# Optimization experiments

Hardware: AMD Instinct MI355X
Metric: run time of the kernel (lower is better)

## Reference

```python
import jax, jax.numpy as jnp
import numpy as np

EMBED_DIM = 1024
K_DIM = 64
NUM_HEADS = 16


def setup_inputs() -> dict:
    key = jax.random.key(0)
    kx, kq, kk, kv, kw = jax.random.split(key, 5)
    x = jax.random.normal(kx, (4, 2048, EMBED_DIM), dtype=jnp.float32)
    # per-head weights stacked along a leading head axis (torch.randn init)
    wq = jax.random.normal(kq, (NUM_HEADS, EMBED_DIM, K_DIM), dtype=jnp.float32)
    wk = jax.random.normal(kk, (NUM_HEADS, EMBED_DIM, K_DIM), dtype=jnp.float32)
    wv = jax.random.normal(kv, (NUM_HEADS, EMBED_DIM, K_DIM), dtype=jnp.float32)
    w = jax.random.normal(kw, (NUM_HEADS * K_DIM, EMBED_DIM), dtype=jnp.float32)
    return {"x": x, "wq": wq, "wk": wk, "wv": wv, "w": w}


def reference(x, wq, wk, wv, w):
    # x: [B,S,D]; wq/wk/wv: [H,D,K]; w: [H*K, D]
    q = jnp.einsum('bsd,hdk->bhsk', x, wq)
    k = jnp.einsum('bsd,hdk->bhsk', x, wk)
    v = jnp.einsum('bsd,hdk->bhsk', x, wv)
    scale = 1.0 / jnp.sqrt(jnp.asarray(K_DIM, x.dtype))
    scores = jnp.einsum('bhsk,bhtk->bhst', q, k) * scale  # [B,H,S,S]
    attn = jax.nn.softmax(scores, axis=-1)
    ctx = jnp.einsum('bhst,bhtk->bhsk', attn, v)  # [B,H,S,K]
    B, H, S, K = ctx.shape
    # concat heads along last dim in head order (matches torch.cat of per-head outs)
    heads = jnp.transpose(ctx, (0, 2, 1, 3)).reshape(B, S, H * K)
    return jnp.matmul(heads, w)  # [B,S,D]
```

## Files before the change

kernel.cpp:

```cpp
#include <hip/hip_runtime.h>
#include <hip/hip_bf16.h>
#include <math.h>

#define EMBED 1024
#define KD 64
#define NH 16
#define SEQ 2048
#define BATCH 4
#define BH (BATCH * NH)
#define NTOK ((size_t)BH * SEQ * KD)

typedef float4 f4;
typedef unsigned short u16;
typedef __attribute__((ext_vector_type(8))) short v8s;
typedef __attribute__((ext_vector_type(4))) float v4f;

__device__ __forceinline__ u16 f2bf(float f) {
    unsigned u = __float_as_uint(f);
    unsigned r = (u + 0x7fffu + ((u >> 16) & 1u)) >> 16;
    return (u16)r;
}
__device__ __forceinline__ float bf2f(u16 h) {
    return __uint_as_float(((unsigned)h) << 16);
}

__device__ __forceinline__ void gload_lds16(const void* g, void* l) {
    __builtin_amdgcn_global_load_lds(
        (const __attribute__((address_space(1))) unsigned int*)g,
        (__attribute__((address_space(3))) unsigned int*)l, 16, 0, 0);
}

__global__ __launch_bounds__(256)
void convert_all_kernel(const float* __restrict__ x,
                        const float* __restrict__ wq, const float* __restrict__ wk,
                        const float* __restrict__ wv, const float* __restrict__ w,
                        u16* __restrict__ xh, u16* __restrict__ xl,
                        u16* __restrict__ Wth, u16* __restrict__ Wtl,
                        u16* __restrict__ OWth, u16* __restrict__ OWtl)
{
    int b = blockIdx.x;
    if (b < 8192) {
        size_t i = ((size_t)b * 256 + threadIdx.x) * 4;
        f4 v = *(const f4*)(x + i);
        u16 h0 = f2bf(v.x), h1 = f2bf(v.y), h2 = f2bf(v.z), h3 = f2bf(v.w);
        u16 l0 = f2bf(v.x - bf2f(h0)), l1 = f2bf(v.y - bf2f(h1));
        u16 l2 = f2bf(v.z - bf2f(h2)), l3 = f2bf(v.w - bf2f(h3));
        uint2 H, L;
        H.x = (unsigned)h0 | ((unsigned)h1 << 16);
        H.y = (unsigned)h2 | ((unsigned)h3 << 16);
        L.x = (unsigned)l0 | ((unsigned)l1 << 16);
        L.y = (unsigned)l2 | ((unsigned)l3 << 16);
        *(uint2*)(xh + i) = H;
        *(uint2*)(xl + i) = L;
    } else if (b < 8192 + 3072) {
        int n = b - 8192;
        int mat = n >> 10, nin = n & 1023, h = nin >> 6, c = nin & 63;
        const float* __restrict__ ws = (mat == 0) ? wq : (mat == 1) ? wk : wv;
        float sc = (mat == 0) ? (0.125f * 1.4426950408889634f) : 1.0f;
        for (int d = threadIdx.x; d < EMBED; d += 256) {
            float f = ws[((size_t)h * EMBED + d) * KD + c] * sc;
            u16 hi = f2bf(f);
            u16 lo = f2bf(f - bf2f(hi));
            Wth[(size_t)n * EMBED + d] = hi;
            Wtl[(size_t)n * EMBED + d] = lo;
        }
    } else {
        int n = b - 11264;
        for (int k = threadIdx.x; k < EMBED; k += 256) {
            float f = w[(size_t)k * EMBED + n];
            u16 hi = f2bf(f);
            u16 lo = f2bf(f - bf2f(hi));
            OWth[(size_t)n * EMBED + k] = hi;
            OWtl[(size_t)n * EMBED + k] = lo;
        }
    }
}

__global__ __launch_bounds__(256)
void qkv_mfma_kernel(const u16* __restrict__ xh, const u16* __restrict__ xl,
                     const u16* __restrict__ Wth, const u16* __restrict__ Wtl,
                     u16* __restrict__ Qhi, u16* __restrict__ Qlo,
                     u16* __restrict__ Khi, u16* __restrict__ Klo,
                     u16* __restrict__ Vt)
{
    __shared__ u16 sAh[128 * 64];
    __shared__ u16 sAl[128 * 64];
    __shared__ u16 sBh[128 * 64];
    __shared__ u16 sBl[128 * 64];
    const int tid = threadIdx.x;
    const int lane = tid & 63, wid = tid >> 6;
    const int lm = lane & 15, lq = lane >> 4;
    const int wm = wid & 1, wn = wid >> 1;
    const int m0 = blockIdx.y * 128;
    const int n0 = blockIdx.x * 128;
    const bool three = (n0 < 2048);

    v4f acc[4][4];
#pragma unroll
    for (int mt = 0; mt < 4; ++mt)
#pragma unroll
        for (int nt = 0; nt < 4; ++nt)
            acc[mt][nt] = (v4f){0.f, 0.f, 0.f, 0.f};

    const int srow = wid * 32 + (lane >> 3);
    const int sblk = (lane & 7) ^ (lane >> 3);

    for (int k0 = 0; k0 < EMBED; k0 += 64) {
        __syncthreads();
#pragma unroll
        for (int i = 0; i < 4; ++i) {
            int row = srow + i * 8;
            size_t gA = (((size_t)(m0 + row)) << 10) + k0 + sblk * 8;
            size_t gB = (((size_t)(n0 + row)) << 10) + k0 + sblk * 8;
            int lo = (wid * 32 + i * 8) * 128;
            gload_lds16((const char*)xh + gA * 2, (char*)sAh + lo);
            gload_lds16((const char*)Wth + gB * 2, (char*)sBh + lo);
            if (three) {
                gload_lds16((const char*)xl + gA * 2, (char*)sAl + lo);
                gload_lds16((const char*)Wtl + gB * 2, (char*)sBl + lo);
            }
        }
        asm volatile("s_waitcnt vmcnt(0)" ::: "memory");
        __syncthreads();

#pragma unroll
        for (int kks = 0; kks < 2; ++kks) {
            v8s ah[4], bh[4];
            const int ba = ((kks * 4 + lq) ^ (lm & 7)) * 8;
#pragma unroll
            for (int t = 0; t < 4; ++t) {
                int ra = wm * 64 + t * 16 + lm;
                int rb = wn * 64 + t * 16 + lm;
                ah[t] = *(const v8s*)&sAh[ra * 64 + ba];
                bh[t] = *(const v8s*)&sBh[rb * 64 + ba];
            }
            if (three) {
                v8s al[4], bl[4];
#pragma unroll
                for (int t = 0; t < 4; ++t) {
                    int ra = wm * 64 + t * 16 + lm;
                    int rb = wn * 64 + t * 16 + lm;
                    al[t] = *(const v8s*)&sAl[ra * 64 + ba];
                    bl[t] = *(const v8s*)&sBl[rb * 64 + ba];
                }
#pragma unroll
                for (int mt = 0; mt < 4; ++mt)
#pragma unroll
                    for (int nt = 0; nt < 4; ++nt) {
                        acc[mt][nt] = __builtin_amdgcn_mfma_f32_16x16x32_bf16(ah[mt], bh[nt], acc[mt][nt], 0, 0, 0);
                        acc[mt][nt] = __builtin_amdgcn_mfma_f32_16x16x32_bf16(ah[mt], bl[nt], acc[mt][nt], 0, 0, 0);
                        acc[mt][nt] = __builtin_amdgcn_mfma_f32_16x16x32_bf16(al[mt], bh[nt], acc[mt][nt], 0, 0, 0);
                    }
            } else {
#pragma unroll
                for (int mt = 0; mt < 4; ++mt)
#pragma unroll
                    for (int nt = 0; nt < 4; ++nt)
                        acc[mt][nt] = __builtin_amdgcn_mfma_f32_16x16x32_bf16(ah[mt], bh[nt], acc[mt][nt], 0, 0, 0);
            }
        }
    }

    const int mrow0 = m0 + wm * 64;
    const int ncol0 = n0 + wn * 64;
    if (!three) {
#pragma unroll
        for (int mt = 0; mt < 4; ++mt) {
            int sbase = mrow0 + mt * 16 + lq * 4;
            int bb = sbase >> 11, s = sbase & 2047;
#pragma unroll
            for (int nt = 0; nt < 4; ++nt) {
                int nin = (ncol0 + nt * 16 + lm) & 1023;
                int h = nin >> 6, cc = nin & 63;
                int bh_ = bb * NH + h;
                size_t a = ((size_t)bh_ * KD + cc) * SEQ
                         + (size_t)(((((s >> 3) ^ (cc & 7)) << 3)) | (s & 7));
                uint2 u;
                u.x = (unsigned)f2bf(acc[mt][nt][0]) | ((unsigned)f2bf(acc[mt][nt][1]) << 16);
                u.y = (unsigned)f2bf(acc[mt][nt][2]) | ((unsigned)f2bf(acc[mt][nt][3]) << 16);
                *(uint2*)(Vt + a) = u;
            }
        }
    } else {
        const bool isQ = (n0 < 1024);
#pragma unroll
        for (int mt = 0; mt < 4; ++mt) {
            int sbase = mrow0 + mt * 16 + lq * 4;
            int bb = sbase >> 11, sB = sbase & 2047;
#pragma unroll
            for (int nt = 0; nt < 4; ++nt) {
                int nin = (ncol0 + nt * 16 + lm) & 1023;
                int h = nin >> 6, cc = nin & 63;
                int bh_ = bb * NH + h;
#pragma unroll
                for (int r = 0; r < 4; ++r) {
                    int s = sB + r;
                    float f = acc[mt][nt][r];
                    u16 hi = f2bf(f);
                    u16 lo = f2bf(f - bf2f(hi));
                    if (isQ) {
                        size_t a = ((size_t)bh_ * SEQ + s) * KD + cc;
                        Qhi[a] = hi;
                        Qlo[a] = lo;
                    } else {
                        int ccp = ((((cc >> 3) ^ (s & 7)) << 3) | (cc & 7));
                        size_t a = ((size_t)bh_ * SEQ + s) * KD + ccp;
                        Khi[a] = hi;
                        Klo[a] = lo;
                    }
                }
            }
        }
    }
}

#define PSTRIDE 72

__global__ __launch_bounds__(256)
void attn_kernel(const u16* __restrict__ Qhi, const u16* __restrict__ Qlo,
                 const u16* __restrict__ Khi, const u16* __restrict__ Klo,
                 const u16* __restrict__ Vt,  u16* __restrict__ headsb)
{
    __shared__ u16 sKhi[64 * 64];
    __shared__ u16 sKlo[64 * 64];
    __shared__ u16 sVt[64 * 64];
    __shared__ u16 sPs[128 * PSTRIDE];

    const int tid = threadIdx.x;
    const int lane = tid & 63, wid = tid >> 6;
    const int lm = lane & 15, lq = lane >> 4;
    const int q0 = blockIdx.x * 128;
    const int bh = blockIdx.y;
    const int bb = bh >> 4, h = bh & 15;

    v8s qh[2][2], ql[2][2];
#pragma unroll
    for (int qt = 0; qt < 2; ++qt)
#pragma unroll
        for (int kk = 0; kk < 2; ++kk) {
            size_t g = ((size_t)bh * SEQ + q0 + wid * 32 + qt * 16 + lm) * KD
                     + kk * 32 + lq * 8;
            qh[qt][kk] = *(const v8s*)(Qhi + g);
            ql[qt][kk] = *(const v8s*)(Qlo + g);
        }

    v8s vones;
#pragma unroll
    for (int i = 0; i < 8; ++i) vones[i] = (short)0x3F80;

    int bpaddr[4];
#pragma unroll
    for (int r = 0; r < 4; ++r)
        bpaddr[r] = (((lane & 48) | (lq * 4 + r)) << 2);

    v4f ctx[2][4], lcol[2];
    float mrun[2];
#pragma unroll
    for (int qt = 0; qt < 2; ++qt) {
        lcol[qt] = (v4f){0.f, 0.f, 0.f, 0.f};
        mrun[qt] = -INFINITY;
#pragma unroll
        for (int nt = 0; nt < 4; ++nt)
            ctx[qt][nt] = (v4f){0.f, 0.f, 0.f, 0.f};
    }

    const size_t kbase = (size_t)bh * SEQ * KD;

    for (int t0 = 0; t0 < SEQ; t0 += 64) {
        __syncthreads();
        {
            const char* gk1 = (const char*)(Khi + kbase + (size_t)t0 * KD);
            const char* gk2 = (const char*)(Klo + kbase + (size_t)t0 * KD);
            int off = wid * 2048;
#pragma unroll
            for (int i = 0; i < 2; ++i) {
                int o = off + i * 1024;
                gload_lds16(gk1 + o + lane * 16, (char*)sKhi + o);
                gload_lds16(gk2 + o + lane * 16, (char*)sKlo + o);
            }
        }
#pragma unroll
        for (int i = 0; i < 2; ++i) {
            int row = wid * 16 + i * 8;
            const char* gv = (const char*)(Vt + ((size_t)bh * KD + row + (lane >> 3)) * SEQ + t0)
                           + (lane & 7) * 16;
            gload_lds16(gv, (char*)sVt + row * 128);
        }
        asm volatile("s_waitcnt vmcnt(0)" ::: "memory");
        __syncthreads();

        v4f sc[4][2];
#pragma unroll
        for (int kt = 0; kt < 4; ++kt)
#pragma unroll
            for (int qt = 0; qt < 2; ++qt)
                sc[kt][qt] = (v4f){0.f, 0.f, 0.f, 0.f};
#pragma unroll
        for (int kk = 0; kk < 2; ++kk) {
#pragma unroll
            for (int kt = 0; kt < 4; ++kt) {
                int key = kt * 16 + lm;
                int blk = (kk * 4 + lq) ^ (key & 7);
                v8s kh16 = *(const v8s*)&sKhi[key * 64 + blk * 8];
                v8s kl16 = *(const v8s*)&sKlo[key * 64 + blk * 8];
#pragma unroll
                for (int qt = 0; qt < 2; ++qt) {
                    sc[kt][qt] = __builtin_amdgcn_mfma_f32_16x16x32_bf16(kh16, qh[qt][kk], sc[kt][qt], 0, 0, 0);
                    sc[kt][qt] = __builtin_amdgcn_mfma_f32_16x16x32_bf16(kl16, qh[qt][kk], sc[kt][qt], 0, 0, 0);
                    sc[kt][qt] = __builtin_amdgcn_mfma_f32_16x16x32_bf16(kh16, ql[qt][kk], sc[kt][qt], 0, 0, 0);
                }
            }
        }

        float aq[2];
#pragma unroll
        for (int qt = 0; qt < 2; ++qt) {
            float m0v = fmaxf(fmaxf(sc[0][qt][0], sc[0][qt][1]), fmaxf(sc[0][qt][2], sc[0][qt][3]));
            float m1v = fmaxf(fmaxf(sc[1][qt][0], sc[1][qt][1]), fmaxf(sc[1][qt][2], sc[1][qt][3]));
            float m2v = fmaxf(fmaxf(sc[2][qt][0], sc[2][qt][1]), fmaxf(sc[2][qt][2], sc[2][qt][3]));
            float m3v = fmaxf(fmaxf(sc[3][qt][0], sc[3][qt][1]), fmaxf(sc[3][qt][2], sc[3][qt][3]));
            float mx = fmaxf(fmaxf(m0v, m1v), fmaxf(m2v, m3v));
            mx = fmaxf(mx, __shfl_xor(mx, 16));
            mx = fmaxf(mx, __shfl_xor(mx, 32));
            float mold = mrun[qt];
            float mnew = fmaxf(mold, mx);
            aq[qt] = __builtin_amdgcn_exp2f(mold - mnew);
            mrun[qt] = mnew;
            u16* pbase = &sPs[(wid * 32 + qt * 16 + lm) * PSTRIDE];
#pragma unroll
            for (int kt = 0; kt < 4; ++kt) {
                unsigned u0 = __float_as_uint(__builtin_amdgcn_exp2f(sc[kt][qt][0] - mnew));
                unsigned u1 = __float_as_uint(__builtin_amdgcn_exp2f(sc[kt][qt][1] - mnew));
                unsigned u2 = __float_as_uint(__builtin_amdgcn_exp2f(sc[kt][qt][2] - mnew));
                unsigned u3 = __float_as_uint(__builtin_amdgcn_exp2f(sc[kt][qt][3] - mnew));
                uint2 pk;
                pk.x = __builtin_amdgcn_perm(u1, u0, 0x07060302);
                pk.y = __builtin_amdgcn_perm(u3, u2, 0x07060302);
                *(uint2*)&pbase[kt * 16 + lq * 4] = pk;
            }
        }

#pragma unroll
        for (int qt = 0; qt < 2; ++qt) {
#pragma unroll
            for (int r = 0; r < 4; ++r) {
                float ar = __uint_as_float(
                    __builtin_amdgcn_ds_bpermute(bpaddr[r], __float_as_uint(aq[qt])));
                lcol[qt][r] *= ar;
#pragma unroll
                for (int nt = 0; nt < 4; ++nt)
                    ctx[qt][nt][r] *= ar;
            }
        }

#pragma unroll
        for (int kk2 = 0; kk2 < 2; ++kk2) {
            v8s a[2];
#pragma unroll
            for (int qt = 0; qt < 2; ++qt)
                a[qt] = *(const v8s*)&sPs[(wid * 32 + qt * 16 + lm) * PSTRIDE + kk2 * 32 + lq * 8];
#pragma unroll
            for (int nt = 0; nt < 4; ++nt) {
                int hd = nt * 16 + lm;
                int blk = (kk2 * 4 + lq) ^ (hd & 7);
                v8s b = *(const v8s*)&sVt[hd * 64 + blk * 8];
#pragma unroll
                for (int qt = 0; qt < 2; ++qt)
                    ctx[qt][nt] = __builtin_amdgcn_mfma_f32_16x16x32_bf16(a[qt], b, ctx[qt][nt], 0, 0, 0);
            }
#pragma unroll
            for (int qt = 0; qt < 2; ++qt)
                lcol[qt] = __builtin_amdgcn_mfma_f32_16x16x32_bf16(a[qt], vones, lcol[qt], 0, 0, 0);
        }
    }

#pragma unroll
    for (int qt = 0; qt < 2; ++qt)
#pragma unroll
        for (int r = 0; r < 4; ++r) {
            int row = q0 + wid * 32 + qt * 16 + lq * 4 + r;
            float inv = 1.0f / lcol[qt][r];
            u16* dst = headsb + ((size_t)bb * SEQ + row) * EMBED + h * KD;
#pragma unroll
            for (int nt = 0; nt < 4; ++nt)
                dst[nt * 16 + lm] = f2bf(ctx[qt][nt][r] * inv);
        }
}

__global__ __launch_bounds__(256)
void out_mfma_kernel(const u16* __restrict__ headsb,
                     const u16* __restrict__ OWth, const u16* __restrict__ OWtl,
                     float* __restrict__ out)
{
    __shared__ u16 sA[128 * 64];
    __shared__ u16 sBh[128 * 64];
    __shared__ u16 sBl[128 * 64];
    const int tid = threadIdx.x;
    const int lane = tid & 63, wid = tid >> 6;
    const int lm = lane & 15, lq = lane >> 4;
    const int wm = wid & 1, wn = wid >> 1;
    const int m0 = blockIdx.y * 128;
    const int n0 = blockIdx.x * 128;

    v4f acc[4][4];
#pragma unroll
    for (int mt = 0; mt < 4; ++mt)
#pragma unroll
        for (int nt = 0; nt < 4; ++nt)
            acc[mt][nt] = (v4f){0.f, 0.f, 0.f, 0.f};

    const int srow = wid * 32 + (lane >> 3);
    const int sblk = (lane & 7) ^ (lane >> 3);

    for (int k0 = 0; k0 < EMBED; k0 += 64) {
        __syncthreads();
#pragma unroll
        for (int i = 0; i < 4; ++i) {
            int row = srow + i * 8;
            size_t gA = (((size_t)(m0 + row)) << 10) + k0 + sblk * 8;
            size_t gB = (((size_t)(n0 + row)) << 10) + k0 + sblk * 8;
            int lo = (wid * 32 + i * 8) * 128;
            gload_lds16((const char*)headsb + gA * 2, (char*)sA + lo);
            gload_lds16((const char*)OWth + gB * 2, (char*)sBh + lo);
            gload_lds16((const char*)OWtl + gB * 2, (char*)sBl + lo);
        }
        asm volatile("s_waitcnt vmcnt(0)" ::: "memory");
        __syncthreads();

#pragma unroll
        for (int kks = 0; kks < 2; ++kks) {
            const int ba = ((kks * 4 + lq) ^ (lm & 7)) * 8;
            v8s ah[4], bh[4], bl[4];
#pragma unroll
            for (int t = 0; t < 4; ++t) {
                int ra = wm * 64 + t * 16 + lm;
                int rb = wn * 64 + t * 16 + lm;
                ah[t] = *(const v8s*)&sA[ra * 64 + ba];
                bh[t] = *(const v8s*)&sBh[rb * 64 + ba];
                bl[t] = *(const v8s*)&sBl[rb * 64 + ba];
            }
#pragma unroll
            for (int mt = 0; mt < 4; ++mt)
#pragma unroll
                for (int nt = 0; nt < 4; ++nt) {
                    acc[mt][nt] = __builtin_amdgcn_mfma_f32_16x16x32_bf16(ah[mt], bh[nt], acc[mt][nt], 0, 0, 0);
                    acc[mt][nt] = __builtin_amdgcn_mfma_f32_16x16x32_bf16(ah[mt], bl[nt], acc[mt][nt], 0, 0, 0);
                }
        }
    }

    const int mrow0 = m0 + wm * 64;
    const int ncol0 = n0 + wn * 64;
#pragma unroll
    for (int mt = 0; mt < 4; ++mt) {
        int sbase = mrow0 + mt * 16 + lq * 4;
#pragma unroll
        for (int nt = 0; nt < 4; ++nt) {
            int n = ncol0 + nt * 16 + lm;
#pragma unroll
            for (int r = 0; r < 4; ++r)
                out[(size_t)(sbase + r) * EMBED + n] = acc[mt][nt][r];
        }
    }
}

extern "C" void kernel_launch(void* const* d_in, const int* in_sizes, int n_in,
                              void* d_out, int out_size, void* d_ws, size_t ws_size,
                              hipStream_t stream) {
    const float* x  = (const float*)d_in[0];
    const float* wq = (const float*)d_in[1];
    const float* wk = (const float*)d_in[2];
    const float* wv = (const float*)d_in[3];
    const float* w  = (const float*)d_in[4];
    float* out = (float*)d_out;

    u16* Qhi = (u16*)d_ws;
    u16* Qlo = Qhi + NTOK;
    u16* Khi = Qlo + NTOK;
    u16* Klo = Khi + NTOK;
    u16* Vt  = Klo + NTOK;
    u16* xh  = Vt + NTOK;
    u16* xl  = xh + NTOK;
    u16* Wth = xl + NTOK;
    u16* Wtl = Wth + (size_t)3072 * 1024;
    u16* OWth = Wtl + (size_t)3072 * 1024;
    u16* OWtl = OWth + (size_t)1024 * 1024;
    u16* headsb = xh;

    convert_all_kernel<<<12288, 256, 0, stream>>>(x, wq, wk, wv, w,
                                                  xh, xl, Wth, Wtl, OWth, OWtl);

    dim3 g1(24, 64);
    qkv_mfma_kernel<<<g1, 256, 0, stream>>>(xh, xl, Wth, Wtl, Qhi, Qlo, Khi, Klo, Vt);

    dim3 g2(SEQ / 128, BH);
    attn_kernel<<<g2, 256, 0, stream>>>(Qhi, Qlo, Khi, Klo, Vt, headsb);

    dim3 g3(8, 64);
    out_mfma_kernel<<<g3, 256, 0, stream>>>(headsb, OWth, OWtl, out);
}
```

Before: 431.0 us.

## Shrink QKV M-tile, swizzle P buffer, reorder attention grid and add occupancy hint

The QKV projection kernel drops its M tile from 128 to 64 rows, doubling the grid so more blocks can fill the CUs, at the cost of reloading the B tile more often. In the attention kernel the padded P scratch buffer (stride 72) becomes an unpadded 64-wide buffer with an XOR swizzle, which cuts LDS use while aiming to avoid bank conflicts. The attention grid axes are swapped so consecutive blocks cover different batch-heads, and launch_bounds(256,4) is added to push for higher occupancy, which may cause register spilling.

```diff
diff --git a/kernel.cpp b/kernel.cpp
--- a/kernel.cpp
+++ b/kernel.cpp
@@ -83,68 +83,78 @@
                      u16* __restrict__ Khi, u16* __restrict__ Klo,
                      u16* __restrict__ Vt)
 {
-    __shared__ u16 sAh[128 * 64];
-    __shared__ u16 sAl[128 * 64];
+    __shared__ u16 sAh[64 * 64];
+    __shared__ u16 sAl[64 * 64];
     __shared__ u16 sBh[128 * 64];
     __shared__ u16 sBl[128 * 64];
     const int tid = threadIdx.x;
     const int lane = tid & 63, wid = tid >> 6;
     const int lm = lane & 15, lq = lane >> 4;
     const int wm = wid & 1, wn = wid >> 1;
-    const int m0 = blockIdx.y * 128;
+    const int m0 = blockIdx.y * 64;
     const int n0 = blockIdx.x * 128;
     const bool three = (n0 < 2048);
 
-    v4f acc[4][4];
-#pragma unroll
-    for (int mt = 0; mt < 4; ++mt)
+    v4f acc[2][4];
+#pragma unroll
+    for (int mt = 0; mt < 2; ++mt)
 #pragma unroll
         for (int nt = 0; nt < 4; ++nt)
             acc[mt][nt] = (v4f){0.f, 0.f, 0.f, 0.f};
 
-    const int srow = wid * 32 + (lane >> 3);
     const int sblk = (lane & 7) ^ (lane >> 3);
 
     for (int k0 = 0; k0 < EMBED; k0 += 64) {
         __syncthreads();
 #pragma unroll
+        for (int i = 0; i < 2; ++i) {
+            int row = wid * 16 + i * 8 + (lane >> 3);
+            size_t gA = (((size_t)(m0 + row)) << 10) + k0 + sblk * 8;
+            int lo = (wid * 16 + i * 8) * 128;
+            gload_lds16((const char*)xh + gA * 2, (char*)sAh + lo);
+            if (three)
+                gload_lds16((const char*)xl + gA * 2, (char*)sAl + lo);
+        }
+#pragma unroll
         for (int i = 0; i < 4; ++i) {
-            int row = srow + i * 8;
-            size_t gA = (((size_t)(m0 + row)) << 10) + k0 + sblk * 8;
+            int row = wid * 32 + i * 8 + (lane >> 3);
             size_t gB = (((size_t)(n0 + row)) << 10) + k0 + sblk * 8;
             int lo = (wid * 32 + i * 8) * 128;
-            gload_lds16((const char*)xh + gA * 2, (char*)sAh + lo);
             gload_lds16((const char*)Wth + gB * 2, (char*)sBh + lo);
-            if (three) {
-                gload_lds16((const char*)xl + gA * 2, (char*)sAl + lo);
+            if (three)
                 gload_lds16((const char*)Wtl + gB * 2, (char*)sBl + lo);
-            }
         }
         asm volatile("s_waitcnt vmcnt(0)" ::: "memory");
         __syncthreads();
 
 #pragma unroll
         for (int kks = 0; kks < 2; ++kks) {
-            v8s ah[4], bh[4];
             const int ba = ((kks * 4 + lq) ^ (lm & 7)) * 8;
+            v8s ah[2], bh[4];
+#pragma unroll
+            for (int t = 0; t < 2; ++t) {
+                int ra = wm * 32 + t * 16 + lm;
+                ah[t] = *(const v8s*)&sAh[ra * 64 + ba];
+            }
 #pragma unroll
             for (int t = 0; t < 4; ++t) {
-                int ra = wm * 64 + t * 16 + lm;
                 int rb = wn * 64 + t * 16 + lm;
-                ah[t] = *(const v8s*)&sAh[ra * 64 + ba];
                 bh[t] = *(const v8s*)&sBh[rb * 64 + ba];
             }
             if (three) {
-                v8s al[4], bl[4];
+                v8s al[2], bl[4];
+#pragma unroll
+                for (int t = 0; t < 2; ++t) {
+                    int ra = wm * 32 + t * 16 + lm;
+                    al[t] = *(const v8s*)&sAl[ra * 64 + ba];
+                }
 #pragma unroll
                 for (int t = 0; t < 4; ++t) {
-                    int ra = wm * 64 + t * 16 + lm;
                     int rb = wn * 64 + t * 16 + lm;
-                    al[t] = *(const v8s*)&sAl[ra * 64 + ba];
                     bl[t] = *(const v8s*)&sBl[rb * 64 + ba];
                 }
 #pragma unroll
-                for (int mt = 0; mt < 4; ++mt)
+                for (int mt = 0; mt < 2; ++mt)
 #pragma unroll
                     for (int nt = 0; nt < 4; ++nt) {
                         acc[mt][nt] = __builtin_amdgcn_mfma_f32_16x16x32_bf16(ah[mt], bh[nt], acc[mt][nt], 0, 0, 0);
@@ -153,7 +163,7 @@
                     }
             } else {
 #pragma unroll
-                for (int mt = 0; mt < 4; ++mt)
+                for (int mt = 0; mt < 2; ++mt)
 #pragma unroll
                     for (int nt = 0; nt < 4; ++nt)
                         acc[mt][nt] = __builtin_amdgcn_mfma_f32_16x16x32_bf16(ah[mt], bh[nt], acc[mt][nt], 0, 0, 0);
@@ -161,11 +171,11 @@
         }
     }
 
-    const int mrow0 = m0 + wm * 64;
+    const int mrow0 = m0 + wm * 32;
     const int ncol0 = n0 + wn * 64;
     if (!three) {
 #pragma unroll
-        for (int mt = 0; mt < 4; ++mt) {
+        for (int mt = 0; mt < 2; ++mt) {
             int sbase = mrow0 + mt * 16 + lq * 4;
             int bb = sbase >> 11, s = sbase & 2047;
 #pragma unroll
@@ -184,7 +194,7 @@
     } else {
         const bool isQ = (n0 < 1024);
 #pragma unroll
-        for (int mt = 0; mt < 4; ++mt) {
+        for (int mt = 0; mt < 2; ++mt) {
             int sbase = mrow0 + mt * 16 + lq * 4;
             int bb = sbase >> 11, sB = sbase & 2047;
 #pragma unroll
@@ -214,9 +224,7 @@
     }
 }
 
-#define PSTRIDE 72
-
-__global__ __launch_bounds__(256)
+__global__ __launch_bounds__(256, 4)
 void attn_kernel(const u16* __restrict__ Qhi, const u16* __restrict__ Qlo,
                  const u16* __restrict__ Khi, const u16* __restrict__ Klo,
                  const u16* __restrict__ Vt,  u16* __restrict__ headsb)
@@ -224,13 +232,13 @@
     __shared__ u16 sKhi[64 * 64];
     __shared__ u16 sKlo[64 * 64];
     __shared__ u16 sVt[64 * 64];
-    __shared__ u16 sPs[128 * PSTRIDE];
+    __shared__ u16 sPs[128 * 64];
 
     const int tid = threadIdx.x;
     const int lane = tid & 63, wid = tid >> 6;
     const int lm = lane & 15, lq = lane >> 4;
-    const int q0 = blockIdx.x * 128;
-    const int bh = blockIdx.y;
+    const int bh = blockIdx.x;
+    const int q0 = blockIdx.y * 128;
     const int bb = bh >> 4, h = bh & 15;
 
     v8s qh[2][2], ql[2][2];
@@ -326,7 +334,9 @@
             float mnew = fmaxf(mold, mx);
             aq[qt] = __builtin_amdgcn_exp2f(mold - mnew);
             mrun[qt] = mnew;
-            u16* pbase = &sPs[(wid * 32 + qt * 16 + lm) * PSTRIDE];
+            int row = wid * 32 + qt * 16 + lm;
+            u16* pbase = &sPs[row * 64];
+            int rsw = (row & 7);
 #pragma unroll
             for (int kt = 0; kt < 4; ++kt) {
                 unsigned u0 = __float_as_uint(__builtin_amdgcn_exp2f(sc[kt][qt][0] - mnew));
@@ -336,7 +346,8 @@
                 uint2 pk;
                 pk.x = __builtin_amdgcn_perm(u1, u0, 0x07060302);
                 pk.y = __builtin_amdgcn_perm(u3, u2, 0x07060302);
-                *(uint2*)&pbase[kt * 16 + lq * 4] = pk;
+                int bkp = (kt * 2 + (lq >> 1)) ^ rsw;
+                *(uint2*)&pbase[bkp * 8 + (lq & 1) * 4] = pk;
             }
         }
 
@@ -357,8 +368,11 @@
         for (int kk2 = 0; kk2 < 2; ++kk2) {
             v8s a[2];
 #pragma unroll
-            for (int qt = 0; qt < 2; ++qt)
-                a[qt] = *(const v8s*)&sPs[(wid * 32 + qt * 16 + lm) * PSTRIDE + kk2 * 32 + lq * 8];
+            for (int qt = 0; qt < 2; ++qt) {
+                int row = wid * 32 + qt * 16 + lm;
+                int bkr = (kk2 * 4 + lq) ^ (row & 7);
+                a[qt] = *(const v8s*)&sPs[row * 64 + bkr * 8];
+            }
 #pragma unroll
             for (int nt = 0; nt < 4; ++nt) {
                 int hd = nt * 16 + lm;
@@ -490,10 +504,10 @@
     convert_all_kernel<<<12288, 256, 0, stream>>>(x, wq, wk, wv, w,
                                                   xh, xl, Wth, Wtl, OWth, OWtl);
 
-    dim3 g1(24, 64);
+    dim3 g1(24, 128);
     qkv_mfma_kernel<<<g1, 256, 0, stream>>>(xh, xl, Wth, Wtl, Qhi, Qlo, Khi, Klo, Vt);
 
-    dim3 g2(SEQ / 128, BH);
+    dim3 g2(BH, SEQ / 128);
     attn_kernel<<<g2, 256, 0, stream>>>(Qhi, Qlo, Khi, Klo, Vt, headsb);
 
     dim3 g3(8, 64);
```

Measured after the change: 512.0 us. +18.8%, slower.
